# Performance work log

Hardware: AMD Instinct MI355X
Metric: run time of the kernel (lower is better)

## Reference

```python
import jax, jax.numpy as jnp
import numpy as np

L, D, H, F, V = 6, 512, 8, 2048, 32000
HD = D // H  # head dim = 64

def _p(key, shape, scale=0.02):
    return (jax.random.normal(key, shape, dtype=jnp.float32) * scale)

def setup_inputs() -> dict:
    key = jax.random.key(0)
    ks = iter(jax.random.split(key, 64))
    N, S = 2, 2048
    src = jax.random.randint(next(ks), (N, S), 0, V, dtype=jnp.int64)
    src_mask = jnp.ones((N, 1, 1, S), dtype=jnp.int32)
    inp = {
        'src': src, 'src_mask': src_mask,
        'emb': _p(next(ks), (V, D)),
        'Wq': _p(next(ks), (L, HD, HD)), 'bq': jnp.zeros((L, HD), jnp.float32),
        'Wk': _p(next(ks), (L, HD, HD)), 'bk': jnp.zeros((L, HD), jnp.float32),
        'Wv': _p(next(ks), (L, HD, HD)), 'bv': jnp.zeros((L, HD), jnp.float32),
        'Wo': _p(next(ks), (L, D, D)),   'bo': jnp.zeros((L, D), jnp.float32),
        'W1': _p(next(ks), (L, F, D)),   'b1': jnp.zeros((L, F), jnp.float32),
        'W2': _p(next(ks), (L, D, F)),   'b2': jnp.zeros((L, D), jnp.float32),
        'ln1_g': jnp.ones((L, D), jnp.float32), 'ln1_b': jnp.zeros((L, D), jnp.float32),
        'ln2_g': jnp.ones((L, D), jnp.float32), 'ln2_b': jnp.zeros((L, D), jnp.float32),
    }
    return inp

def _layer_norm(x, g, b, eps=1e-5):
    m = jnp.mean(x, axis=-1, keepdims=True)
    v = jnp.mean(jnp.square(x - m), axis=-1, keepdims=True)
    return (x - m) / jnp.sqrt(v + eps) * g + b

def _attention(x, mask, Wq, bq, Wk, bk, Wv, bv, Wo, bo):
    N, S, _ = x.shape
    xh = x.reshape(N, S, H, HD)                      # [n, s, h, d]
    # shared per-head projections (Linear(head_dim, head_dim), torch y = x W^T + b)
    Q = jnp.einsum('nshd,ed->nshe', xh, Wq) + bq
    K = jnp.einsum('nshd,ed->nshe', xh, Wk) + bk
    Vv = jnp.einsum('nshd,ed->nshe', xh, Wv) + bv
    energy = jnp.einsum('nqhd,nkhd->nhqk', Q, K)     # [n, h, q, k]
    energy = jnp.where(mask == 0, jnp.float32(-1e10), energy)
    # NOTE: original scales by sqrt(hid_dim), not sqrt(head_dim)
    attn = jax.nn.softmax(energy / jnp.sqrt(jnp.float32(D)), axis=-1)
    out = jnp.einsum('nhql,nlhd->nqhd', attn, Vv).reshape(N, S, D)
    return out @ Wo.T + bo

def reference(src, src_mask, emb, Wq, bq, Wk, bk, Wv, bv, Wo, bo,
              W1, b1, W2, b2, ln1_g, ln1_b, ln2_g, ln2_b):
    h = emb[src] * jnp.sqrt(jnp.float32(D))          # [N, S, D]
    for l in range(L):
        a = _attention(h, src_mask, Wq[l], bq[l], Wk[l], bk[l],
                       Wv[l], bv[l], Wo[l], bo[l])
        h = _layer_norm(h + a, ln1_g[l], ln1_b[l])
        ff = jax.nn.relu(h @ W1[l].T + b1[l]) @ W2[l].T + b2[l]
        h = _layer_norm(h + ff, ln2_g[l], ln2_b[l])
    return h
```

## Files before the change

### kernel.cpp

```cpp
#include <hip/hip_runtime.h>
#include <hip/hip_bf16.h>


#define NS_TOK 4096
#define DMODEL 512
#define NHEAD 8
#define HDIM 64
#define FFDIM 2048
#define SEQ 2048
#define NB 2

typedef __hip_bfloat16 bf16;
typedef __attribute__((ext_vector_type(8))) short short8;
typedef __attribute__((ext_vector_type(4))) float floatx4;

__device__ __forceinline__ float bf2f(bf16 x) { return __bfloat162float(x); }
__device__ __forceinline__ bf16 f2bf(float x) { return __float2bfloat16(x); }
__device__ __forceinline__ short bfbits(float x) {
    bf16 h = __float2bfloat16(x);
    return *reinterpret_cast<short*>(&h);
}
__device__ __forceinline__ float2 bf2x2(unsigned int u) {
    float2 r;
    r.x = __uint_as_float(u << 16);
    r.y = __uint_as_float(u & 0xffff0000u);
    return r;
}
__device__ __forceinline__ void gl2lds16(const void* g, void* l) {
    __builtin_amdgcn_global_load_lds(
        (const __attribute__((address_space(1))) void*)g,
        (__attribute__((address_space(3))) void*)l, 16, 0, 0);
}

__global__ __launch_bounds__(256) void k_conv(const float* __restrict__ src,
                                              bf16* __restrict__ dst, int count) {
    int i = (blockIdx.x * 256 + threadIdx.x) * 8;
    if (i >= count) return;
    float4 f0 = *(const float4*)(src + i);
    float4 f1 = *(const float4*)(src + i + 4);
    short8 sv;
    sv[0] = bfbits(f0.x); sv[1] = bfbits(f0.y);
    sv[2] = bfbits(f0.z); sv[3] = bfbits(f0.w);
    sv[4] = bfbits(f1.x); sv[5] = bfbits(f1.y);
    sv[6] = bfbits(f1.z); sv[7] = bfbits(f1.w);
    *(short8*)(dst + i) = sv;
}

__global__ __launch_bounds__(256) void k_embed(const int* __restrict__ src,
                                               const float* __restrict__ emb,
                                               float* __restrict__ h,
                                               bf16* __restrict__ hb) {
    int row = blockIdx.x;
    int t = threadIdx.x;
    int tok = src[row];
    const float* e = emb + (size_t)tok * DMODEL;
    float v0 = e[t] * 22.62741699796952f;
    float v1 = e[t + 256] * 22.62741699796952f;
    h[(size_t)row * DMODEL + t] = v0;
    h[(size_t)row * DMODEL + t + 256] = v1;
    hb[(size_t)row * DMODEL + t] = f2bf(v0);
    hb[(size_t)row * DMODEL + t + 256] = f2bf(v1);
}

__global__ __launch_bounds__(256) void k_qkv(const bf16* __restrict__ hb,
    const float* __restrict__ Wq, const float* __restrict__ bq,
    const float* __restrict__ Wk, const float* __restrict__ bk,
    const float* __restrict__ Wv, const float* __restrict__ bv,
    bf16* __restrict__ Qo, bf16* __restrict__ Ko, bf16* __restrict__ Vt) {
    __shared__ __align__(16) short Xs[64 * 72];
    __shared__ __align__(16) short Ws3[3][64 * 72];
    int t = threadIdx.x, lane = t & 63, w = t >> 6;
    int l15 = lane & 15, quad = lane >> 4;
    int tok0 = blockIdx.x * 64, hh = blockIdx.y;
    int n = tok0 >> 11, s0loc = tok0 & 2047;
    const float QSC = 0.044194173824159216f * 1.44269504088896341f;
    const float* Ws[3] = {Wq, Wk, Wv};
    const float* Bs[3] = {bq, bk, bv};

    #pragma unroll
    for (int i = 0; i < 2; ++i) {
        int idx = t + i * 256;
        int row = idx >> 3, g = idx & 7;
        *(uint4*)&Xs[row * 72 + g * 8] =
            *(const uint4*)(hb + (size_t)(tok0 + row) * DMODEL + hh * HDIM + g * 8);
    }
    #pragma unroll
    for (int tn = 0; tn < 3; ++tn)
        #pragma unroll
        for (int i = 0; i < 2; ++i) {
            int idx = t + i * 256;
            int row = idx >> 3, g = idx & 7;
            const float* srcp = Ws[tn] + row * HDIM + g * 8;
            float4 f0 = *(const float4*)srcp;
            float4 f1 = *(const float4*)(srcp + 4);
            short8 sv;
            sv[0] = bfbits(f0.x); sv[1] = bfbits(f0.y);
            sv[2] = bfbits(f0.z); sv[3] = bfbits(f0.w);
            sv[4] = bfbits(f1.x); sv[5] = bfbits(f1.y);
            sv[6] = bfbits(f1.z); sv[7] = bfbits(f1.w);
            *(short8*)&Ws3[tn][row * 72 + g * 8] = sv;
        }
    __syncthreads();
    short8 aq[2];
    aq[0] = *(short8*)&Xs[(w * 16 + l15) * 72 + quad * 8];
    aq[1] = *(short8*)&Xs[(w * 16 + l15) * 72 + 32 + quad * 8];

    #pragma unroll
    for (int tn = 0; tn < 3; ++tn) {
        floatx4 acc[4];
        #pragma unroll
        for (int fj = 0; fj < 4; ++fj)
            #pragma unroll
            for (int r = 0; r < 4; ++r) acc[fj][r] = 0.f;
        #pragma unroll
        for (int ks = 0; ks < 2; ++ks)
            #pragma unroll
            for (int fj = 0; fj < 4; ++fj) {
                short8 bfrag = *(short8*)&Ws3[tn][(fj * 16 + l15) * 72 + ks * 32 + quad * 8];
                acc[fj] = __builtin_amdgcn_mfma_f32_16x16x32_bf16(aq[ks], bfrag, acc[fj], 0, 0, 0);
            }
        #pragma unroll
        for (int fj = 0; fj < 4; ++fj) {
            int col = fj * 16 + l15;
            float bias = Bs[tn][col];
            if (tn < 2) {
                bf16* O = (tn == 0) ? Qo : Ko;
                float sc = (tn == 0) ? QSC : 1.f;
                #pragma unroll
                for (int r = 0; r < 4; ++r) {
                    int tok = tok0 + w * 16 + quad * 4 + r;
                    O[(size_t)tok * DMODEL + hh * HDIM + col] = f2bf((acc[fj][r] + bias) * sc);
                }
            } else {
                short4 pk;
                pk.x = bfbits(acc[fj][0] + bias); pk.y = bfbits(acc[fj][1] + bias);
                pk.z = bfbits(acc[fj][2] + bias); pk.w = bfbits(acc[fj][3] + bias);
                int sl = s0loc + w * 16 + quad * 4;
                *(short4*)(Vt + ((size_t)((n * NHEAD + hh) * HDIM + col)) * SEQ + sl) = pk;
            }
        }
    }
}

__global__ __launch_bounds__(256) void k_attn(const bf16* __restrict__ Qb,
                                              const bf16* __restrict__ Kb,
                                              const bf16* __restrict__ Vt,
                                              const int* __restrict__ mask,
                                              bf16* __restrict__ PoA,
                                              bf16* __restrict__ PoB,
                                              float* __restrict__ Mm,
                                              float* __restrict__ Ll,
                                              int ns_l2) {
    __shared__ __align__(16) short QPs[64 * 72];
    __shared__ __align__(16) short Ks[64 * 72];
    __shared__ __align__(16) short Vs[80 * 72];
    int t = threadIdx.x, lane = t & 63, w = t >> 6;
    int l15 = lane & 15, quad = lane >> 4;
    int q0 = blockIdx.x * 64, hh = blockIdx.y;
    int z = blockIdx.z;
    int n = z >> ns_l2, sp = z & ((1 << ns_l2) - 1);
    size_t tokbase = (size_t)n * SEQ;
    size_t vbase = ((size_t)(n * NHEAD + hh) * HDIM) * SEQ;

    #pragma unroll
    for (int i = 0; i < 2; ++i) {
        int idx = t + 256 * i;
        int row = idx >> 3, q = idx & 7;
        *(uint4*)&QPs[row * 72 + q * 8] =
            *(const uint4*)(Qb + (tokbase + q0 + row) * DMODEL + hh * HDIM + q * 8);
    }
    for (int j = t; j < 16 * 72; j += 256) Vs[64 * 72 + j] = 0;
    if (t < 64) Vs[64 * 72 + t] = (short)0x3F80;
    __syncthreads();
    short8 aq[2];
    aq[0] = *(short8*)&QPs[(w * 16 + l15) * 72 + quad * 8];
    aq[1] = *(short8*)&QPs[(w * 16 + l15) * 72 + 32 + quad * 8];

    floatx4 accO[5];
    float mold[4];
    #pragma unroll
    for (int fn = 0; fn < 5; ++fn)
        #pragma unroll
        for (int r = 0; r < 4; ++r) accO[fn][r] = 0.f;
    #pragma unroll
    for (int r = 0; r < 4; ++r) mold[r] = -1.0e38f;

    int kquota = SEQ >> ns_l2;
    int kbeg = sp * kquota, kend = kbeg + kquota;
    for (int k0 = kbeg; k0 < kend; k0 += 64) {
        __syncthreads();
        #pragma unroll
        for (int i = 0; i < 2; ++i) {
            int idx = t + 256 * i;
            int row = idx >> 3, q = idx & 7;
            *(uint4*)&Ks[row * 72 + q * 8] =
                *(const uint4*)(Kb + (tokbase + k0 + row) * DMODEL + hh * HDIM + q * 8);
            *(uint4*)&Vs[row * 72 + q * 8] =
                *(const uint4*)(Vt + vbase + (size_t)row * SEQ + k0 + q * 8);
        }
        __syncthreads();
        floatx4 accS[4];
        #pragma unroll
        for (int fj = 0; fj < 4; ++fj)
            #pragma unroll
            for (int r = 0; r < 4; ++r) accS[fj][r] = 0.f;
        #pragma unroll
        for (int ks = 0; ks < 2; ++ks)
            #pragma unroll
            for (int fj = 0; fj < 4; ++fj) {
                short8 bk = *(short8*)&Ks[(fj * 16 + l15) * 72 + ks * 32 + quad * 8];
                accS[fj] = __builtin_amdgcn_mfma_f32_16x16x32_bf16(aq[ks], bk, accS[fj], 0, 0, 0);
            }
        #pragma unroll
        for (int fj = 0; fj < 4; ++fj) {
            int mk = mask[n * SEQ + k0 + fj * 16 + l15];
            #pragma unroll
            for (int r = 0; r < 4; ++r)
                accS[fj][r] = mk ? accS[fj][r] : -1.0e9f;
        }
        float al[4];
        short* Ps = &QPs[w * 1152];
        #pragma unroll
        for (int r = 0; r < 4; ++r) {
            float mx = fmaxf(fmaxf(accS[0][r], accS[1][r]), fmaxf(accS[2][r], accS[3][r]));
            mx = fmaxf(mx, __shfl_xor(mx, 1, 64));
            mx = fmaxf(mx, __shfl_xor(mx, 2, 64));
            mx = fmaxf(mx, __shfl_xor(mx, 4, 64));
            mx = fmaxf(mx, __shfl_xor(mx, 8, 64));
            float mn = fmaxf(mold[r], mx);
            al[r] = exp2f(mold[r] - mn);
            mold[r] = mn;
            #pragma unroll
            for (int fj = 0; fj < 4; ++fj) {
                float p = exp2f(accS[fj][r] - mn);
                Ps[(quad * 4 + r) * 72 + fj * 16 + l15] = bfbits(p);
            }
        }
        #pragma unroll
        for (int fn = 0; fn < 5; ++fn)
            #pragma unroll
            for (int r = 0; r < 4; ++r) accO[fn][r] *= al[r];
        #pragma unroll
        for (int ks = 0; ks < 2; ++ks) {
            short8 ap = *(short8*)&Ps[l15 * 72 + ks * 32 + quad * 8];
            #pragma unroll
            for (int fn = 0; fn < 5; ++fn) {
                short8 bv = *(short8*)&Vs[(fn * 16 + l15) * 72 + ks * 32 + quad * 8];
                accO[fn] = __builtin_amdgcn_mfma_f32_16x16x32_bf16(ap, bv, accO[fn], 0, 0, 0);
            }
        }
    }
    bf16* Pob = (sp < 2) ? PoA : PoB;
    #pragma unroll
    for (int r = 0; r < 4; ++r) {
        float ls = __shfl(accO[4][r], lane & 48);
        int row = q0 + w * 16 + quad * 4 + r;
        size_t gtok = tokbase + row;
        bf16* dst = Pob + ((size_t)(sp & 1) * NS_TOK + gtok) * DMODEL + hh * HDIM;
        #pragma unroll
        for (int fn = 0; fn < 4; ++fn)
            dst[fn * 16 + l15] = f2bf(accO[fn][r]);
        if (l15 == 0) {
            Mm[((size_t)sp * NS_TOK + gtok) * NHEAD + hh] = mold[r];
            Ll[((size_t)sp * NS_TOK + gtok) * NHEAD + hh] = ls;
        }
    }
}

__global__ __launch_bounds__(256) void k_comb(const bf16* __restrict__ PoA,
    const bf16* __restrict__ PoB, const float* __restrict__ Mm,
    const float* __restrict__ Ll, bf16* __restrict__ Ab, int nsplit) {
    int tok = blockIdx.x * 4 + (threadIdx.x >> 6);
    int lane = threadIdx.x & 63;
    int hh = lane >> 3;
    float m = -1.0e38f;
    for (int s = 0; s < nsplit; ++s)
        m = fmaxf(m, Mm[((size_t)s * NS_TOK + tok) * NHEAD + hh]);
    float L = 0.f, wgt[4];
    for (int s = 0; s < nsplit; ++s) {
        wgt[s] = exp2f(Mm[((size_t)s * NS_TOK + tok) * NHEAD + hh] - m);
        L += Ll[((size_t)s * NS_TOK + tok) * NHEAD + hh] * wgt[s];
    }
    float inv = 1.f / L;
    float acc[8] = {0.f, 0.f, 0.f, 0.f, 0.f, 0.f, 0.f, 0.f};
    for (int s = 0; s < nsplit; ++s) {
        const bf16* base = ((s < 2) ? PoA : PoB) +
                           ((size_t)(s & 1) * NS_TOK + tok) * DMODEL + lane * 8;
        uint4 u = *(const uint4*)base;
        const unsigned int* p = (const unsigned int*)&u;
        #pragma unroll
        for (int j = 0; j < 4; ++j) {
            float2 f = bf2x2(p[j]);
            acc[j * 2]     += f.x * wgt[s];
            acc[j * 2 + 1] += f.y * wgt[s];
        }
    }
    bf16* dst = Ab + (size_t)tok * DMODEL + lane * 8;
    #pragma unroll
    for (int j = 0; j < 8; ++j) dst[j] = f2bf(acc[j] * inv);
}

template<int MT, int NT, bool RELU>
__global__ __launch_bounds__(256) void k_gemm_f(const bf16* __restrict__ A,
    const bf16* __restrict__ W, const float* __restrict__ bias, int K, int N,
    const float* __restrict__ resid, float* __restrict__ outF, bf16* __restrict__ outB) {
    constexpr int FI = MT / 32;
    constexpr int FJ = NT / 32;
    __shared__ __align__(16) short As[MT * 32];
    __shared__ __align__(16) short Bs[NT * 32];
    int t = threadIdx.x, lane = t & 63, w = t >> 6;
    int m0 = blockIdx.x * MT, n0 = blockIdx.y * NT;
    int wrow = (w >> 1) * (MT / 2), wcol = (w & 1) * (NT / 2);
    int quad = lane >> 4, mrow = lane & 15;
    int lr = lane >> 2, lc = (lane & 3) * 8;
    floatx4 acc[FI][FJ];
    #pragma unroll
    for (int fi = 0; fi < FI; ++fi)
        #pragma unroll
        for (int fj = 0; fj < FJ; ++fj)
            #pragma unroll
            for (int r = 0; r < 4; ++r) acc[fi][fj][r] = 0.f;

    for (int k0 = 0; k0 < K; k0 += 32) {
        __syncthreads();
        #pragma unroll
        for (int i = 0; i < MT / 64; ++i) {
            int rbase = (i * 4 + w) * 16;
            gl2lds16(A + (size_t)(m0 + rbase + lr) * K + k0 + lc, &As[rbase * 32]);
        }
        #pragma unroll
        for (int i = 0; i < NT / 64; ++i) {
            int rbase = (i * 4 + w) * 16;
            gl2lds16(W + (size_t)(n0 + rbase + lr) * K + k0 + lc, &Bs[rbase * 32]);
        }
        __syncthreads();
        short8 af[FI], bfr[FJ];
        #pragma unroll
        for (int fi = 0; fi < FI; ++fi)
            af[fi] = *(short8*)&As[(wrow + fi * 16 + mrow) * 32 + quad * 8];
        #pragma unroll
        for (int fj = 0; fj < FJ; ++fj)
            bfr[fj] = *(short8*)&Bs[(wcol + fj * 16 + mrow) * 32 + quad * 8];
        #pragma unroll
        for (int fi = 0; fi < FI; ++fi)
            #pragma unroll
            for (int fj = 0; fj < FJ; ++fj)
                acc[fi][fj] = __builtin_amdgcn_mfma_f32_16x16x32_bf16(
                    af[fi], bfr[fj], acc[fi][fj], 0, 0, 0);
    }
    #pragma unroll
    for (int fi = 0; fi < FI; ++fi)
        #pragma unroll
        for (int fj = 0; fj < FJ; ++fj) {
            int col = n0 + wcol + fj * 16 + mrow;
            float bv = bias[col];
            #pragma unroll
            for (int r = 0; r < 4; ++r) {
                int row = m0 + wrow + fi * 16 + quad * 4 + r;
                float v = acc[fi][fj][r] + bv;
                if (RELU) {
                    outB[(size_t)row * N + col] = f2bf(fmaxf(v, 0.f));
                } else {
                    outF[(size_t)row * N + col] = v + resid[(size_t)row * N + col];
                }
            }
        }
}

template<int MT, int NT>
__global__ __launch_bounds__(256) void k_gemm_sk(const bf16* __restrict__ A,
    const bf16* __restrict__ W, int K, int N,
    float* __restrict__ out0, float* __restrict__ out1) {
    constexpr int FI = MT / 32;
    constexpr int FJ = NT / 32;
    __shared__ __align__(16) short As[MT * 32];
    __shared__ __align__(16) short Bs[NT * 32];
    int t = threadIdx.x, lane = t & 63, w = t >> 6;
    int m0 = blockIdx.x * MT, n0 = blockIdx.y * NT;
    int wrow = (w >> 1) * (MT / 2), wcol = (w & 1) * (NT / 2);
    int quad = lane >> 4, mrow = lane & 15;
    int lr = lane >> 2, lc = (lane & 3) * 8;
    floatx4 acc[FI][FJ];
    #pragma unroll
    for (int fi = 0; fi < FI; ++fi)
        #pragma unroll
        for (int fj = 0; fj < FJ; ++fj)
            #pragma unroll
            for (int r = 0; r < 4; ++r) acc[fi][fj][r] = 0.f;

    int kh = K >> 1;
    int kbeg = blockIdx.z * kh;
    for (int k0 = kbeg; k0 < kbeg + kh; k0 += 32) {
        __syncthreads();
        #pragma unroll
        for (int i = 0; i < MT / 64; ++i) {
            int rbase = (i * 4 + w) * 16;
            gl2lds16(A + (size_t)(m0 + rbase + lr) * K + k0 + lc, &As[rbase * 32]);
        }
        #pragma unroll
        for (int i = 0; i < NT / 64; ++i) {
            int rbase = (i * 4 + w) * 16;
            gl2lds16(W + (size_t)(n0 + rbase + lr) * K + k0 + lc, &Bs[rbase * 32]);
        }
        __syncthreads();
        short8 af[FI], bfr[FJ];
        #pragma unroll
        for (int fi = 0; fi < FI; ++fi)
            af[fi] = *(short8*)&As[(wrow + fi * 16 + mrow) * 32 + quad * 8];
        #pragma unroll
        for (int fj = 0; fj < FJ; ++fj)
            bfr[fj] = *(short8*)&Bs[(wcol + fj * 16 + mrow) * 32 + quad * 8];
        #pragma unroll
        for (int fi = 0; fi < FI; ++fi)
            #pragma unroll
            for (int fj = 0; fj < FJ; ++fj)
                acc[fi][fj] = __builtin_amdgcn_mfma_f32_16x16x32_bf16(
                    af[fi], bfr[fj], acc[fi][fj], 0, 0, 0);
    }
    float* out = blockIdx.z ? out1 : out0;
    #pragma unroll
    for (int fi = 0; fi < FI; ++fi)
        #pragma unroll
        for (int fj = 0; fj < FJ; ++fj) {
            int col = n0 + wcol + fj * 16 + mrow;
            #pragma unroll
            for (int r = 0; r < 4; ++r) {
                int row = m0 + wrow + fi * 16 + quad * 4 + r;
                out[(size_t)row * N + col] = acc[fi][fj][r];
            }
        }
}

template<int MT, bool RELU>
__global__ __launch_bounds__(256) void k_gemm(const bf16* __restrict__ A,
    const float* __restrict__ Wf, const float* __restrict__ bias, int K, int N,
    const float* __restrict__ resid, float* __restrict__ outF, bf16* __restrict__ outB) {
    constexpr int FI = 4;
    constexpr int FJ = (MT == 128) ? 4 : 2;
    __shared__ short As[MT * 40];
    __shared__ short Bs[128 * 40];
    int t = threadIdx.x, lane = t & 63, w = t >> 6;
    int m0 = blockIdx.x * MT, n0 = blockIdx.y * 128;
    int wrow = (MT == 128) ? (w >> 1) * 64 : 0;
    int wcol = (MT == 128) ? (w & 1) * 64 : w * 32;
    int quad = lane >> 4, mrow = lane & 15;
    floatx4 acc[FI][FJ];
    #pragma unroll
    for (int fi = 0; fi < FI; ++fi)
        #pragma unroll
        for (int fj = 0; fj < FJ; ++fj)
            #pragma unroll
            for (int r = 0; r < 4; ++r) acc[fi][fj][r] = 0.f;
    for (int k0 = 0; k0 < K; k0 += 32) {
        __syncthreads();
        #pragma unroll
        for (int i = 0; i < MT / 64; ++i) {
            int idx = t + i * 256;
            int row = idx >> 2, q = idx & 3;
            uint4 u = *(const uint4*)(A + (size_t)(m0 + row) * K + k0 + q * 8);
            *(uint4*)&As[row * 40 + q * 8] = u;
        }
        #pragma unroll
        for (int i = 0; i < 2; ++i) {
            int idx = t + i * 256;
            int row = idx >> 2, q = idx & 3;
            const float* src = Wf + (size_t)(n0 + row) * K + k0 + q * 8;
            float4 f0 = *(const float4*)src;
            float4 f1 = *(const float4*)(src + 4);
            short8 sv;
            sv[0] = bfbits(f0.x); sv[1] = bfbits(f0.y);
            sv[2] = bfbits(f0.z); sv[3] = bfbits(f0.w);
            sv[4] = bfbits(f1.x); sv[5] = bfbits(f1.y);
            sv[6] = bfbits(f1.z); sv[7] = bfbits(f1.w);
            *(short8*)&Bs[row * 40 + q * 8] = sv;
        }
        __syncthreads();
        short8 af[FI], bfr[FJ];
        #pragma unroll
        for (int fi = 0; fi < FI; ++fi)
            af[fi] = *(short8*)&As[(wrow + fi * 16 + mrow) * 40 + quad * 8];
        #pragma unroll
        for (int fj = 0; fj < FJ; ++fj)
            bfr[fj] = *(short8*)&Bs[(wcol + fj * 16 + mrow) * 40 + quad * 8];
        #pragma unroll
        for (int fi = 0; fi < FI; ++fi)
            #pragma unroll
            for (int fj = 0; fj < FJ; ++fj)
                acc[fi][fj] = __builtin_amdgcn_mfma_f32_16x16x32_bf16(
                    af[fi], bfr[fj], acc[fi][fj], 0, 0, 0);
    }
    #pragma unroll
    for (int fi = 0; fi < FI; ++fi)
        #pragma unroll
        for (int fj = 0; fj < FJ; ++fj) {
            int col = n0 + wcol + fj * 16 + mrow;
            float bv = bias[col];
            #pragma unroll
            for (int r = 0; r < 4; ++r) {
                int row = m0 + wrow + fi * 16 + quad * 4 + r;
                float v = acc[fi][fj][r] + bv;
                if (RELU) {
                    outB[(size_t)row * N + col] = f2bf(fmaxf(v, 0.f));
                } else {
                    outF[(size_t)row * N + col] = v + resid[(size_t)row * N + col];
                }
            }
        }
}

__global__ __launch_bounds__(256) void k_ln(const float* __restrict__ P,
    const float* __restrict__ g, const float* __restrict__ b,
    float* __restrict__ outF, bf16* __restrict__ outB) {
    int row = blockIdx.x * 4 + (threadIdx.x >> 6);
    int lane = threadIdx.x & 63;
    const float* p = P + (size_t)row * DMODEL + lane * 8;
    float4 a = *(const float4*)p;
    float4 c = *(const float4*)(p + 4);
    float s = a.x + a.y + a.z + a.w + c.x + c.y + c.z + c.w;
    #pragma unroll
    for (int off = 32; off > 0; off >>= 1) s += __shfl_xor(s, off, 64);
    float mean = s * (1.f / DMODEL);
    float d[8] = {a.x - mean, a.y - mean, a.z - mean, a.w - mean,
                  c.x - mean, c.y - mean, c.z - mean, c.w - mean};
    float vs = 0.f;
    #pragma unroll
    for (int j = 0; j < 8; ++j) vs += d[j] * d[j];
    #pragma unroll
    for (int off = 32; off > 0; off >>= 1) vs += __shfl_xor(vs, off, 64);
    float rstd = rsqrtf(vs * (1.f / DMODEL) + 1e-5f);
    float4 g0 = *(const float4*)(g + lane * 8);
    float4 g1 = *(const float4*)(g + lane * 8 + 4);
    float4 b0 = *(const float4*)(b + lane * 8);
    float4 b1 = *(const float4*)(b + lane * 8 + 4);
    float o[8] = {d[0] * rstd * g0.x + b0.x, d[1] * rstd * g0.y + b0.y,
                  d[2] * rstd * g0.z + b0.z, d[3] * rstd * g0.w + b0.w,
                  d[4] * rstd * g1.x + b1.x, d[5] * rstd * g1.y + b1.y,
                  d[6] * rstd * g1.z + b1.z, d[7] * rstd * g1.w + b1.w};
    float* of = outF + (size_t)row * DMODEL + lane * 8;
    *(float4*)of       = make_float4(o[0], o[1], o[2], o[3]);
    *(float4*)(of + 4) = make_float4(o[4], o[5], o[6], o[7]);
    if (outB) {
        bf16* ob = outB + (size_t)row * DMODEL + lane * 8;
        #pragma unroll
        for (int j = 0; j < 8; ++j) ob[j] = f2bf(o[j]);
    }
}

__global__ __launch_bounds__(256) void k_lncomb(const float* __restrict__ pp0,
    const float* __restrict__ pp1, const float* __restrict__ bias,
    const float* __restrict__ resid, const float* __restrict__ g,
    const float* __restrict__ b, float* __restrict__ outF, bf16* __restrict__ outB) {
    int row = blockIdx.x * 4 + (threadIdx.x >> 6);
    int lane = threadIdx.x & 63;
    size_t idx = (size_t)row * DMODEL + lane * 8;
    float4 a0 = *(const float4*)(pp0 + idx),  a1 = *(const float4*)(pp0 + idx + 4);
    float4 c0 = *(const float4*)(pp1 + idx),  c1 = *(const float4*)(pp1 + idx + 4);
    float4 r0 = *(const float4*)(resid + idx), r1 = *(const float4*)(resid + idx + 4);
    float4 q0 = *(const float4*)(bias + lane * 8), q1 = *(const float4*)(bias + lane * 8 + 4);
    float v[8] = {a0.x + c0.x + r0.x + q0.x, a0.y + c0.y + r0.y + q0.y,
                  a0.z + c0.z + r0.z + q0.z, a0.w + c0.w + r0.w + q0.w,
                  a1.x + c1.x + r1.x + q1.x, a1.y + c1.y + r1.y + q1.y,
                  a1.z + c1.z + r1.z + q1.z, a1.w + c1.w + r1.w + q1.w};
    float s = 0.f;
    #pragma unroll
    for (int j = 0; j < 8; ++j) s += v[j];
    #pragma unroll
    for (int off = 32; off > 0; off >>= 1) s += __shfl_xor(s, off, 64);
    float mean = s * (1.f / DMODEL);
    float vs = 0.f;
    #pragma unroll
    for (int j = 0; j < 8; ++j) { v[j] -= mean; vs += v[j] * v[j]; }
    #pragma unroll
    for (int off = 32; off > 0; off >>= 1) vs += __shfl_xor(vs, off, 64);
    float rstd = rsqrtf(vs * (1.f / DMODEL) + 1e-5f);
    float4 g0 = *(const float4*)(g + lane * 8);
    float4 g1 = *(const float4*)(g + lane * 8 + 4);
    float4 b0 = *(const float4*)(b + lane * 8);
    float4 b1 = *(const float4*)(b + lane * 8 + 4);
    float o[8] = {v[0] * rstd * g0.x + b0.x, v[1] * rstd * g0.y + b0.y,
                  v[2] * rstd * g0.z + b0.z, v[3] * rstd * g0.w + b0.w,
                  v[4] * rstd * g1.x + b1.x, v[5] * rstd * g1.y + b1.y,
                  v[6] * rstd * g1.z + b1.z, v[7] * rstd * g1.w + b1.w};
    float* of = outF + idx;
    *(float4*)of       = make_float4(o[0], o[1], o[2], o[3]);
    *(float4*)(of + 4) = make_float4(o[4], o[5], o[6], o[7]);
    if (outB) {
        bf16* ob = outB + idx;
        #pragma unroll
        for (int j = 0; j < 8; ++j) ob[j] = f2bf(o[j]);
    }
}

extern "C" void kernel_launch(void* const* d_in, const int* in_sizes, int n_in,
                              void* d_out, int out_size, void* d_ws, size_t ws_size,
                              hipStream_t stream) {
    const int*   src  = (const int*)d_in[0];
    const int*   mask = (const int*)d_in[1];
    const float* emb  = (const float*)d_in[2];
    const float* Wq   = (const float*)d_in[3];
    const float* bq   = (const float*)d_in[4];
    const float* Wk   = (const float*)d_in[5];
    const float* bk   = (const float*)d_in[6];
    const float* Wv   = (const float*)d_in[7];
    const float* bv   = (const float*)d_in[8];
    const float* Wo   = (const float*)d_in[9];
    const float* bo   = (const float*)d_in[10];
    const float* W1   = (const float*)d_in[11];
    const float* b1   = (const float*)d_in[12];
    const float* W2   = (const float*)d_in[13];
    const float* b2   = (const float*)d_in[14];
    const float* ln1g = (const float*)d_in[15];
    const float* ln1b = (const float*)d_in[16];
    const float* ln2g = (const float*)d_in[17];
    const float* ln2b = (const float*)d_in[18];

    char* base = (char*)d_ws;
    float* h   = (float*)base;
    float* hbf = (float*)(base + 8388608);
    bf16*  hb  = (bf16*)hbf;
    float* Mm  = hbf;
    float* Ll  = hbf + 4 * NS_TOK * NHEAD;
    float* Pp0 = (float*)(base + 12582912);
    bf16*  Qb  = (bf16*)(base + 20971520);
    bf16*  Kb  = (bf16*)(base + 25165824);
    bf16*  Vt  = (bf16*)(base + 29360128);
    bf16*  Ab  = (bf16*)(base + 33554432);
    bf16*  F1b = Qb;
    bf16*  Wob = (bf16*)(base + 37748736);
    bf16*  W1b = (bf16*)(base + 40894464);
    bf16*  W2b = (bf16*)(base + 53477376);
    float* Pp1 = (float*)(base + 66060288);
    int tier = (ws_size >= 74448896ull) ? 2 : ((ws_size >= 66060288ull) ? 1 : 0);

    if (tier >= 1) {
        k_conv<<<(6 * DMODEL * DMODEL) / 2048, 256, 0, stream>>>(Wo, Wob, 6 * DMODEL * DMODEL);
        k_conv<<<(6 * FFDIM * DMODEL) / 2048, 256, 0, stream>>>(W1, W1b, 6 * FFDIM * DMODEL);
        k_conv<<<(6 * FFDIM * DMODEL) / 2048, 256, 0, stream>>>(W2, W2b, 6 * FFDIM * DMODEL);
    }
    k_embed<<<NS_TOK, 256, 0, stream>>>(src, emb, h, hb);

    int ns_l2 = (tier == 2) ? 2 : 1;
    int nsplit = 1 << ns_l2;
    bf16* PoA = (bf16*)Pp0;
    bf16* PoB = (tier == 2) ? (bf16*)Pp1 : (bf16*)Pp0;

    for (int l = 0; l < 6; ++l) {
        k_qkv<<<dim3(NS_TOK / 64, NHEAD), 256, 0, stream>>>(hb,
            Wq + (size_t)l * HDIM * HDIM, bq + l * HDIM,
            Wk + (size_t)l * HDIM * HDIM, bk + l * HDIM,
            Wv + (size_t)l * HDIM * HDIM, bv + l * HDIM,
            Qb, Kb, Vt);
        k_attn<<<dim3(SEQ / 64, NHEAD, NB * nsplit), 256, 0, stream>>>(
            Qb, Kb, Vt, mask, PoA, PoB, Mm, Ll, ns_l2);
        k_comb<<<NS_TOK / 4, 256, 0, stream>>>(PoA, PoB, Mm, Ll, Ab, nsplit);

        float* lnout = (l == 5) ? (float*)d_out : h;
        bf16* lnoutB = (l == 5) ? nullptr : hb;

        if (tier == 2) {
            k_gemm_sk<64, 128><<<dim3(NS_TOK / 64, DMODEL / 128, 2), 256, 0, stream>>>(
                Ab, Wob + (size_t)l * DMODEL * DMODEL, DMODEL, DMODEL, Pp0, Pp1);
            k_lncomb<<<NS_TOK / 4, 256, 0, stream>>>(Pp0, Pp1, bo + l * DMODEL, h,
                ln1g + l * DMODEL, ln1b + l * DMODEL, h, hb);
            k_gemm_f<128, 128, true><<<dim3(NS_TOK / 128, FFDIM / 128), 256, 0, stream>>>(
                hb, W1b + (size_t)l * FFDIM * DMODEL, b1 + l * FFDIM,
                DMODEL, FFDIM, nullptr, nullptr, F1b);
            k_gemm_sk<64, 128><<<dim3(NS_TOK / 64, DMODEL / 128, 2), 256, 0, stream>>>(
                F1b, W2b + (size_t)l * DMODEL * FFDIM, FFDIM, DMODEL, Pp0, Pp1);
            k_lncomb<<<NS_TOK / 4, 256, 0, stream>>>(Pp0, Pp1, b2 + l * DMODEL, h,
                ln2g + l * DMODEL, ln2b + l * DMODEL, lnout, lnoutB);
        } else if (tier == 1) {
            k_gemm_f<64, 128, false><<<dim3(NS_TOK / 64, DMODEL / 128), 256, 0, stream>>>(
                Ab, Wob + (size_t)l * DMODEL * DMODEL, bo + l * DMODEL,
                DMODEL, DMODEL, h, Pp0, nullptr);
            k_ln<<<NS_TOK / 4, 256, 0, stream>>>(Pp0, ln1g + l * DMODEL, ln1b + l * DMODEL, h, hb);
            k_gemm_f<128, 128, true><<<dim3(NS_TOK / 128, FFDIM / 128), 256, 0, stream>>>(
                hb, W1b + (size_t)l * FFDIM * DMODEL, b1 + l * FFDIM,
                DMODEL, FFDIM, nullptr, nullptr, F1b);
            k_gemm_f<64, 128, false><<<dim3(NS_TOK / 64, DMODEL / 128), 256, 0, stream>>>(
                F1b, W2b + (size_t)l * DMODEL * FFDIM, b2 + l * DMODEL,
                FFDIM, DMODEL, h, Pp0, nullptr);
            k_ln<<<NS_TOK / 4, 256, 0, stream>>>(Pp0, ln2g + l * DMODEL, ln2b + l * DMODEL, lnout, lnoutB);
        } else {
            k_gemm<64, false><<<dim3(NS_TOK / 64, DMODEL / 128), 256, 0, stream>>>(
                Ab, Wo + (size_t)l * DMODEL * DMODEL, bo + l * DMODEL,
                DMODEL, DMODEL, h, Pp0, nullptr);
            k_ln<<<NS_TOK / 4, 256, 0, stream>>>(Pp0, ln1g + l * DMODEL, ln1b + l * DMODEL, h, hb);
            k_gemm<128, true><<<dim3(NS_TOK / 128, FFDIM / 128), 256, 0, stream>>>(
                hb, W1 + (size_t)l * FFDIM * DMODEL, b1 + l * FFDIM,
                DMODEL, FFDIM, nullptr, nullptr, F1b);
            k_gemm<64, false><<<dim3(NS_TOK / 64, DMODEL / 128), 256, 0, stream>>>(
                F1b, W2 + (size_t)l * DMODEL * FFDIM, b2 + l * DMODEL,
                FFDIM, DMODEL, h, Pp0, nullptr);
            k_ln<<<NS_TOK / 4, 256, 0, stream>>>(Pp0, ln2g + l * DMODEL, ln2b + l * DMODEL, lnout, lnoutB);
        }
    }
}
```

Before: 1.010 ms.

## Enlarge attention tiles, transpose V projection, pack P stores, bf16 split-K partials

Attention blocks now cover 128 queries with 512 threads, so each K/V tile loaded to shared memory serves twice as many queries. The V projection is computed transposed (W·Xᵀ), which lets the transposed V output be written as contiguous short4 packs. The softmax P tile is also written as packed short4 stores instead of scalar ones. Split-K GEMM partials are stored in bf16 rather than fp32, halving their memory traffic at the cost of some precision in the residual sum.

```diff
diff --git a/kernel.cpp b/kernel.cpp
--- a/kernel.cpp
+++ b/kernel.cpp
@@ -75,7 +75,6 @@
     int n = tok0 >> 11, s0loc = tok0 & 2047;
     const float QSC = 0.044194173824159216f * 1.44269504088896341f;
     const float* Ws[3] = {Wq, Wk, Wv};
-    const float* Bs[3] = {bq, bk, bv};
 
     #pragma unroll
     for (int i = 0; i < 2; ++i) {
@@ -106,7 +105,8 @@
     aq[1] = *(short8*)&Xs[(w * 16 + l15) * 72 + 32 + quad * 8];
 
     #pragma unroll
-    for (int tn = 0; tn < 3; ++tn) {
+    for (int tn = 0; tn < 2; ++tn) {
+        const float* Bs = (tn == 0) ? bq : bk;
         floatx4 acc[4];
         #pragma unroll
         for (int fj = 0; fj < 4; ++fj)
@@ -119,44 +119,65 @@
                 short8 bfrag = *(short8*)&Ws3[tn][(fj * 16 + l15) * 72 + ks * 32 + quad * 8];
                 acc[fj] = __builtin_amdgcn_mfma_f32_16x16x32_bf16(aq[ks], bfrag, acc[fj], 0, 0, 0);
             }
+        bf16* O = (tn == 0) ? Qo : Ko;
+        float sc = (tn == 0) ? QSC : 1.f;
         #pragma unroll
         for (int fj = 0; fj < 4; ++fj) {
             int col = fj * 16 + l15;
-            float bias = Bs[tn][col];
-            if (tn < 2) {
-                bf16* O = (tn == 0) ? Qo : Ko;
-                float sc = (tn == 0) ? QSC : 1.f;
-                #pragma unroll
-                for (int r = 0; r < 4; ++r) {
-                    int tok = tok0 + w * 16 + quad * 4 + r;
-                    O[(size_t)tok * DMODEL + hh * HDIM + col] = f2bf((acc[fj][r] + bias) * sc);
-                }
-            } else {
-                short4 pk;
-                pk.x = bfbits(acc[fj][0] + bias); pk.y = bfbits(acc[fj][1] + bias);
-                pk.z = bfbits(acc[fj][2] + bias); pk.w = bfbits(acc[fj][3] + bias);
-                int sl = s0loc + w * 16 + quad * 4;
-                *(short4*)(Vt + ((size_t)((n * NHEAD + hh) * HDIM + col)) * SEQ + sl) = pk;
+            float bias = Bs[col];
+            #pragma unroll
+            for (int r = 0; r < 4; ++r) {
+                int tok = tok0 + w * 16 + quad * 4 + r;
+                O[(size_t)tok * DMODEL + hh * HDIM + col] = f2bf((acc[fj][r] + bias) * sc);
             }
         }
     }
-}
-
-__global__ __launch_bounds__(256) void k_attn(const bf16* __restrict__ Qb,
-                                              const bf16* __restrict__ Kb,
-                                              const bf16* __restrict__ Vt,
-                                              const int* __restrict__ mask,
-                                              bf16* __restrict__ PoA,
-                                              bf16* __restrict__ PoB,
-                                              float* __restrict__ Mm,
-                                              float* __restrict__ Ll,
-                                              int ns_l2) {
-    __shared__ __align__(16) short QPs[64 * 72];
+    {
+        short8 av[2];
+        av[0] = *(short8*)&Ws3[2][(w * 16 + l15) * 72 + quad * 8];
+        av[1] = *(short8*)&Ws3[2][(w * 16 + l15) * 72 + 32 + quad * 8];
+        floatx4 acc[4];
+        #pragma unroll
+        for (int fj = 0; fj < 4; ++fj)
+            #pragma unroll
+            for (int r = 0; r < 4; ++r) acc[fj][r] = 0.f;
+        #pragma unroll
+        for (int ks = 0; ks < 2; ++ks)
+            #pragma unroll
+            for (int fj = 0; fj < 4; ++fj) {
+                short8 bx = *(short8*)&Xs[(fj * 16 + l15) * 72 + ks * 32 + quad * 8];
+                acc[fj] = __builtin_amdgcn_mfma_f32_16x16x32_bf16(av[ks], bx, acc[fj], 0, 0, 0);
+            }
+        #pragma unroll
+        for (int r = 0; r < 4; ++r) {
+            int e = w * 16 + quad * 4 + r;
+            float bias = bv[e];
+            short4 pk;
+            pk.x = bfbits(acc[0][r] + bias);
+            pk.y = bfbits(acc[1][r] + bias);
+            pk.z = bfbits(acc[2][r] + bias);
+            pk.w = bfbits(acc[3][r] + bias);
+            *(short4*)(Vt + ((size_t)((n * NHEAD + hh) * HDIM + e)) * SEQ
+                       + s0loc + l15 * 4) = pk;
+        }
+    }
+}
+
+__global__ __launch_bounds__(512, 8) void k_attn(const bf16* __restrict__ Qb,
+                                                 const bf16* __restrict__ Kb,
+                                                 const bf16* __restrict__ Vt,
+                                                 const int* __restrict__ mask,
+                                                 bf16* __restrict__ PoA,
+                                                 bf16* __restrict__ PoB,
+                                                 float* __restrict__ Mm,
+                                                 float* __restrict__ Ll,
+                                                 int ns_l2) {
+    __shared__ __align__(16) short QPs[128 * 72];
     __shared__ __align__(16) short Ks[64 * 72];
     __shared__ __align__(16) short Vs[80 * 72];
     int t = threadIdx.x, lane = t & 63, w = t >> 6;
     int l15 = lane & 15, quad = lane >> 4;
-    int q0 = blockIdx.x * 64, hh = blockIdx.y;
+    int q0 = blockIdx.x * 128, hh = blockIdx.y;
     int z = blockIdx.z;
     int n = z >> ns_l2, sp = z & ((1 << ns_l2) - 1);
     size_t tokbase = (size_t)n * SEQ;
@@ -164,12 +185,12 @@
 
     #pragma unroll
     for (int i = 0; i < 2; ++i) {
-        int idx = t + 256 * i;
+        int idx = t + 512 * i;
         int row = idx >> 3, q = idx & 7;
         *(uint4*)&QPs[row * 72 + q * 8] =
             *(const uint4*)(Qb + (tokbase + q0 + row) * DMODEL + hh * HDIM + q * 8);
     }
-    for (int j = t; j < 16 * 72; j += 256) Vs[64 * 72 + j] = 0;
+    for (int j = t; j < 16 * 72; j += 512) Vs[64 * 72 + j] = 0;
     if (t < 64) Vs[64 * 72 + t] = (short)0x3F80;
     __syncthreads();
     short8 aq[2];
@@ -189,10 +210,8 @@
     int kbeg = sp * kquota, kend = kbeg + kquota;
     for (int k0 = kbeg; k0 < kend; k0 += 64) {
         __syncthreads();
-        #pragma unroll
-        for (int i = 0; i < 2; ++i) {
-            int idx = t + 256 * i;
-            int row = idx >> 3, q = idx & 7;
+        {
+            int row = t >> 3, q = t & 7;
             *(uint4*)&Ks[row * 72 + q * 8] =
                 *(const uint4*)(Kb + (tokbase + k0 + row) * DMODEL + hh * HDIM + q * 8);
             *(uint4*)&Vs[row * 72 + q * 8] =
@@ -230,11 +249,12 @@
             float mn = fmaxf(mold[r], mx);
             al[r] = exp2f(mold[r] - mn);
             mold[r] = mn;
-            #pragma unroll
-            for (int fj = 0; fj < 4; ++fj) {
-                float p = exp2f(accS[fj][r] - mn);
-                Ps[(quad * 4 + r) * 72 + fj * 16 + l15] = bfbits(p);
-            }
+            short4 pk;
+            pk.x = bfbits(exp2f(accS[0][r] - mn));
+            pk.y = bfbits(exp2f(accS[1][r] - mn));
+            pk.z = bfbits(exp2f(accS[2][r] - mn));
+            pk.w = bfbits(exp2f(accS[3][r] - mn));
+            *(short4*)&Ps[(quad * 4 + r) * 72 + l15 * 4] = pk;
         }
         #pragma unroll
         for (int fn = 0; fn < 5; ++fn)
@@ -284,9 +304,9 @@
     float inv = 1.f / L;
     float acc[8] = {0.f, 0.f, 0.f, 0.f, 0.f, 0.f, 0.f, 0.f};
     for (int s = 0; s < nsplit; ++s) {
-        const bf16* base = ((s < 2) ? PoA : PoB) +
-                           ((size_t)(s & 1) * NS_TOK + tok) * DMODEL + lane * 8;
-        uint4 u = *(const uint4*)base;
+        const bf16* basep = ((s < 2) ? PoA : PoB) +
+                            ((size_t)(s & 1) * NS_TOK + tok) * DMODEL + lane * 8;
+        uint4 u = *(const uint4*)basep;
         const unsigned int* p = (const unsigned int*)&u;
         #pragma unroll
         for (int j = 0; j < 4; ++j) {
@@ -370,7 +390,7 @@
 template<int MT, int NT>
 __global__ __launch_bounds__(256) void k_gemm_sk(const bf16* __restrict__ A,
     const bf16* __restrict__ W, int K, int N,
-    float* __restrict__ out0, float* __restrict__ out1) {
+    bf16* __restrict__ out0, bf16* __restrict__ out1) {
     constexpr int FI = MT / 32;
     constexpr int FJ = NT / 32;
     __shared__ __align__(16) short As[MT * 32];
@@ -417,7 +437,7 @@
                 acc[fi][fj] = __builtin_amdgcn_mfma_f32_16x16x32_bf16(
                     af[fi], bfr[fj], acc[fi][fj], 0, 0, 0);
     }
-    float* out = blockIdx.z ? out1 : out0;
+    bf16* out = blockIdx.z ? out1 : out0;
     #pragma unroll
     for (int fi = 0; fi < FI; ++fi)
         #pragma unroll
@@ -426,7 +446,7 @@
             #pragma unroll
             for (int r = 0; r < 4; ++r) {
                 int row = m0 + wrow + fi * 16 + quad * 4 + r;
-                out[(size_t)row * N + col] = acc[fi][fj][r];
+                out[(size_t)row * N + col] = f2bf(acc[fi][fj][r]);
             }
         }
 }
@@ -546,21 +566,28 @@
     }
 }
 
-__global__ __launch_bounds__(256) void k_lncomb(const float* __restrict__ pp0,
-    const float* __restrict__ pp1, const float* __restrict__ bias,
+__global__ __launch_bounds__(256) void k_lncomb(const bf16* __restrict__ pp0,
+    const bf16* __restrict__ pp1, const float* __restrict__ bias,
     const float* __restrict__ resid, const float* __restrict__ g,
     const float* __restrict__ b, float* __restrict__ outF, bf16* __restrict__ outB) {
     int row = blockIdx.x * 4 + (threadIdx.x >> 6);
     int lane = threadIdx.x & 63;
     size_t idx = (size_t)row * DMODEL + lane * 8;
-    float4 a0 = *(const float4*)(pp0 + idx),  a1 = *(const float4*)(pp0 + idx + 4);
-    float4 c0 = *(const float4*)(pp1 + idx),  c1 = *(const float4*)(pp1 + idx + 4);
+    uint4 u0 = *(const uint4*)(pp0 + idx);
+    uint4 u1 = *(const uint4*)(pp1 + idx);
     float4 r0 = *(const float4*)(resid + idx), r1 = *(const float4*)(resid + idx + 4);
     float4 q0 = *(const float4*)(bias + lane * 8), q1 = *(const float4*)(bias + lane * 8 + 4);
-    float v[8] = {a0.x + c0.x + r0.x + q0.x, a0.y + c0.y + r0.y + q0.y,
-                  a0.z + c0.z + r0.z + q0.z, a0.w + c0.w + r0.w + q0.w,
-                  a1.x + c1.x + r1.x + q1.x, a1.y + c1.y + r1.y + q1.y,
-                  a1.z + c1.z + r1.z + q1.z, a1.w + c1.w + r1.w + q1.w};
+    const unsigned int* a0 = (const unsigned int*)&u0;
+    const unsigned int* a1 = (const unsigned int*)&u1;
+    float v[8];
+    #pragma unroll
+    for (int j = 0; j < 4; ++j) {
+        float2 f0 = bf2x2(a0[j]), f1 = bf2x2(a1[j]);
+        v[j * 2]     = f0.x + f1.x;
+        v[j * 2 + 1] = f0.y + f1.y;
+    }
+    v[0] += r0.x + q0.x; v[1] += r0.y + q0.y; v[2] += r0.z + q0.z; v[3] += r0.w + q0.w;
+    v[4] += r1.x + q1.x; v[5] += r1.y + q1.y; v[6] += r1.z + q1.z; v[7] += r1.w + q1.w;
     float s = 0.f;
     #pragma unroll
     for (int j = 0; j < 8; ++j) s += v[j];
@@ -620,7 +647,7 @@
     bf16*  hb  = (bf16*)hbf;
     float* Mm  = hbf;
     float* Ll  = hbf + 4 * NS_TOK * NHEAD;
-    float* Pp0 = (float*)(base + 12582912);
+    char*  P0r = base + 12582912;
     bf16*  Qb  = (bf16*)(base + 20971520);
     bf16*  Kb  = (bf16*)(base + 25165824);
     bf16*  Vt  = (bf16*)(base + 29360128);
@@ -629,7 +656,7 @@
     bf16*  Wob = (bf16*)(base + 37748736);
     bf16*  W1b = (bf16*)(base + 40894464);
     bf16*  W2b = (bf16*)(base + 53477376);
-    float* Pp1 = (float*)(base + 66060288);
+    char*  P1r = base + 66060288;
     int tier = (ws_size >= 74448896ull) ? 2 : ((ws_size >= 66060288ull) ? 1 : 0);
 
     if (tier >= 1) {
@@ -641,8 +668,10 @@
 
     int ns_l2 = (tier == 2) ? 2 : 1;
     int nsplit = 1 << ns_l2;
-    bf16* PoA = (bf16*)Pp0;
-    bf16* PoB = (tier == 2) ? (bf16*)Pp1 : (bf16*)Pp0;
+    bf16* PoA = (bf16*)P0r;
+    bf16* PoB = (tier == 2) ? (bf16*)P1r : (bf16*)P0r;
+    bf16* Pp0 = (bf16*)P0r;
+    bf16* Pp1 = (tier == 2) ? (bf16*)P1r : (bf16*)P0r;
 
     for (int l = 0; l < 6; ++l) {
         k_qkv<<<dim3(NS_TOK / 64, NHEAD), 256, 0, stream>>>(hb,
@@ -650,7 +679,7 @@
             Wk + (size_t)l * HDIM * HDIM, bk + l * HDIM,
             Wv + (size_t)l * HDIM * HDIM, bv + l * HDIM,
             Qb, Kb, Vt);
-        k_attn<<<dim3(SEQ / 64, NHEAD, NB * nsplit), 256, 0, stream>>>(
+        k_attn<<<dim3(SEQ / 128, NHEAD, NB * nsplit), 512, 0, stream>>>(
             Qb, Kb, Vt, mask, PoA, PoB, Mm, Ll, ns_l2);
         k_comb<<<NS_TOK / 4, 256, 0, stream>>>(PoA, PoB, Mm, Ll, Ab, nsplit);
 
@@ -672,27 +701,27 @@
         } else if (tier == 1) {
             k_gemm_f<64, 128, false><<<dim3(NS_TOK / 64, DMODEL / 128), 256, 0, stream>>>(
                 Ab, Wob + (size_t)l * DMODEL * DMODEL, bo + l * DMODEL,
-                DMODEL, DMODEL, h, Pp0, nullptr);
-            k_ln<<<NS_TOK / 4, 256, 0, stream>>>(Pp0, ln1g + l * DMODEL, ln1b + l * DMODEL, h, hb);
+                DMODEL, DMODEL, h, (float*)P0r, nullptr);
+            k_ln<<<NS_TOK / 4, 256, 0, stream>>>((float*)P0r, ln1g + l * DMODEL, ln1b + l * DMODEL, h, hb);
             k_gemm_f<128, 128, true><<<dim3(NS_TOK / 128, FFDIM / 128), 256, 0, stream>>>(
                 hb, W1b + (size_t)l * FFDIM * DMODEL, b1 + l * FFDIM,
                 DMODEL, FFDIM, nullptr, nullptr, F1b);
             k_gemm_f<64, 128, false><<<dim3(NS_TOK / 64, DMODEL / 128), 256, 0, stream>>>(
                 F1b, W2b + (size_t)l * DMODEL * FFDIM, b2 + l * DMODEL,
-                FFDIM, DMODEL, h, Pp0, nullptr);
-            k_ln<<<NS_TOK / 4, 256, 0, stream>>>(Pp0, ln2g + l * DMODEL, ln2b + l * DMODEL, lnout, lnoutB);
+                FFDIM, DMODEL, h, (float*)P0r, nullptr);
+            k_ln<<<NS_TOK / 4, 256, 0, stream>>>((float*)P0r, ln2g + l * DMODEL, ln2b + l * DMODEL, lnout, lnoutB);
         } else {
             k_gemm<64, false><<<dim3(NS_TOK / 64, DMODEL / 128), 256, 0, stream>>>(
                 Ab, Wo + (size_t)l * DMODEL * DMODEL, bo + l * DMODEL,
-                DMODEL, DMODEL, h, Pp0, nullptr);
-            k_ln<<<NS_TOK / 4, 256, 0, stream>>>(Pp0, ln1g + l * DMODEL, ln1b + l * DMODEL, h, hb);
+                DMODEL, DMODEL, h, (float*)P0r, nullptr);
+            k_ln<<<NS_TOK / 4, 256, 0, stream>>>((float*)P0r, ln1g + l * DMODEL, ln1b + l * DMODEL, h, hb);
             k_gemm<128, true><<<dim3(NS_TOK / 128, FFDIM / 128), 256, 0, stream>>>(
                 hb, W1 + (size_t)l * FFDIM * DMODEL, b1 + l * FFDIM,
                 DMODEL, FFDIM, nullptr, nullptr, F1b);
             k_gemm<64, false><<<dim3(NS_TOK / 64, DMODEL / 128), 256, 0, stream>>>(
                 F1b, W2 + (size_t)l * DMODEL * FFDIM, b2 + l * DMODEL,
-                FFDIM, DMODEL, h, Pp0, nullptr);
-            k_ln<<<NS_TOK / 4, 256, 0, stream>>>(Pp0, ln2g + l * DMODEL, ln2b + l * DMODEL, lnout, lnoutB);
-        }
-    }
-}
+                FFDIM, DMODEL, h, (float*)P0r, nullptr);
+            k_ln<<<NS_TOK / 4, 256, 0, stream>>>((float*)P0r, ln2g + l * DMODEL, ln2b + l * DMODEL, lnout, lnoutB);
+        }
+    }
+}
```

Result: slower. 1.188 ms (+17.5%).
